# Optimization experiments

Hardware: AMD Instinct MI355X
Metric: run time of the kernel (lower is better)

The kernel has to match this reference:

```python
import jax, jax.numpy as jnp
import numpy as np

TAU = 0.5

def setup_inputs() -> dict:
    key = jax.random.key(0)
    ks = jax.random.split(key, 9)
    B, N, C, T, R = 32, 196, 768, 10, 16
    s = 0.02
    return {
        "x": jax.random.normal(ks[0], (B, N, C), jnp.float32),
        "W_qkv": jax.random.normal(ks[1], (3 * C, C), jnp.float32) * s,
        "b_qkv": jax.random.normal(ks[2], (3 * C,), jnp.float32) * s,
        "A_q": jax.random.normal(ks[3], (T, R, C), jnp.float32) * s,
        "B_q": jax.random.normal(ks[4], (T, C, R), jnp.float32) * s,
        "A_v": jax.random.normal(ks[5], (T, R, C), jnp.float32) * s,
        "B_v": jax.random.normal(ks[6], (T, C, R), jnp.float32) * s,
        "gate_logits_q": jax.random.normal(ks[7], (T,), jnp.float32),
        "gate_logits_v": jax.random.normal(ks[8], (T,), jnp.float32),
    }

def _fro(w):
    # Frobenius norm per task: w is [T, d1, d2]
    return jnp.sqrt(jnp.sum(w * w, axis=(1, 2)))

def _lora_branch(x, A, B, logits):
    # x: [B,N,C]; A: [T,R,C]; B: [T,C,R]; logits: [T]
    gate = jax.nn.softmax(logits / TAU)                      # soft gumbel gate, eval (no noise)
    scale = gate / (_fro(A) * _fro(B))                       # fuse 1/(||A||*||B||) with gate weight
    tmp = jnp.einsum('bnc,trc->tbnr', x, A)                  # low-rank projections, all tasks batched
    return jnp.einsum('tbnr,tcr,t->bnc', tmp, B, scale)      # up-project + weighted sum over tasks

def reference(x, W_qkv, b_qkv, A_q, B_q, A_v, B_v, gate_logits_q, gate_logits_v):
    C = x.shape[-1]
    qkv = jnp.einsum('bnc,dc->bnd', x, W_qkv) + b_qkv        # [B,N,3C]
    new_q = _lora_branch(x, A_q, B_q, gate_logits_q)
    new_v = _lora_branch(x, A_v, B_v, gate_logits_v)
    qkv = qkv.at[:, :, :C].add(new_q)
    qkv = qkv.at[:, :, 2 * C:].add(new_v)
    return qkv
```

## Files before the change

### kernel.cpp

```cpp
#include <hip/hip_runtime.h>

#define TAU_INV 2.0f

typedef unsigned short u16;
typedef short bf16x8 __attribute__((ext_vector_type(8)));
typedef float f32x4 __attribute__((ext_vector_type(4)));
typedef u16 u16x4v __attribute__((ext_vector_type(4)));
typedef u16 u16x8v __attribute__((ext_vector_type(8)));

typedef __attribute__((address_space(1))) const void GASV;
typedef __attribute__((address_space(3))) void LASV;
#define GLOAD16(gp, lp) __builtin_amdgcn_global_load_lds((GASV*)(gp), (LASV*)(lp), 16, 0, 0)

__device__ __forceinline__ u16 f2bf(float f) {
  unsigned u = __float_as_uint(f);
  u += 0x7FFFu + ((u >> 16) & 1u);
  return (u16)(u >> 16);
}

__global__ __launch_bounds__(256) void k_scales(
    const float* __restrict__ Aq, const float* __restrict__ Bq,
    const float* __restrict__ Av, const float* __restrict__ Bv,
    const float* __restrict__ lq, const float* __restrict__ lv,
    float* __restrict__ scales) {
  const int br = blockIdx.x / 10, t = blockIdx.x % 10;
  const float* __restrict__ A = br ? Av : Aq;
  const float* __restrict__ B = br ? Bv : Bq;
  const float* __restrict__ lg = br ? lv : lq;
  const int tid = threadIdx.x;
  const float4* A4 = (const float4*)(A + t * 12288);
  const float4* B4 = (const float4*)(B + t * 12288);
  float sA = 0.f, sB = 0.f;
  for (int i = tid; i < 3072; i += 256) {
    float4 a = A4[i];
    float4 b = B4[i];
    sA += a.x * a.x + a.y * a.y + a.z * a.z + a.w * a.w;
    sB += b.x * b.x + b.y * b.y + b.z * b.z + b.w * b.w;
  }
  for (int off = 32; off; off >>= 1) {
    sA += __shfl_down(sA, off);
    sB += __shfl_down(sB, off);
  }
  __shared__ float rA[4], rB[4];
  if ((tid & 63) == 0) { rA[tid >> 6] = sA; rB[tid >> 6] = sB; }
  __syncthreads();
  if (tid == 0) {
    sA = rA[0] + rA[1] + rA[2] + rA[3];
    sB = rB[0] + rB[1] + rB[2] + rB[3];
    float mx = -1e30f;
    for (int j = 0; j < 10; ++j) mx = fmaxf(mx, lg[j] * TAU_INV);
    float den = 0.f, num = 0.f;
    for (int j = 0; j < 10; ++j) {
      float e = __expf(lg[j] * TAU_INV - mx);
      den += e;
      if (j == t) num = e;
    }
    scales[br * 16 + t] = (num / den) * rsqrtf(sA) * rsqrtf(sB);
  }
}

__global__ __launch_bounds__(256) void k_xcvt(const float* __restrict__ x,
                                              u16* __restrict__ xb) {
  const int i = (blockIdx.x * 256 + threadIdx.x) * 8;
  float4 v0 = *(const float4*)(x + i);
  float4 v1 = *(const float4*)(x + i + 4);
  u16x8v o;
  o[0] = f2bf(v0.x); o[1] = f2bf(v0.y); o[2] = f2bf(v0.z); o[3] = f2bf(v0.w);
  o[4] = f2bf(v1.x); o[5] = f2bf(v1.y); o[6] = f2bf(v1.z); o[7] = f2bf(v1.w);
  *(u16x8v*)(xb + i) = o;
}

__global__ __launch_bounds__(256) void k_wmid(const float* __restrict__ W,
                                              u16* __restrict__ Weff) {
  const int i = 589824 + (blockIdx.x * 256 + threadIdx.x) * 8;
  float4 v0 = *(const float4*)(W + i);
  float4 v1 = *(const float4*)(W + i + 4);
  u16x8v o;
  o[0] = f2bf(v0.x); o[1] = f2bf(v0.y); o[2] = f2bf(v0.z); o[3] = f2bf(v0.w);
  o[4] = f2bf(v1.x); o[5] = f2bf(v1.y); o[6] = f2bf(v1.z); o[7] = f2bf(v1.w);
  *(u16x8v*)(Weff + i) = o;
}

__global__ __launch_bounds__(256) void k_dwgemm(
    const float* __restrict__ Aq, const float* __restrict__ Bq,
    const float* __restrict__ Av, const float* __restrict__ Bv,
    const float* __restrict__ W, const float* __restrict__ scales,
    u16* __restrict__ Weff) {
  const int bid = blockIdx.x;
  const int br = bid / 36, t36 = bid % 36;
  const int tm = t36 / 6, tn = t36 % 6;
  const float* __restrict__ A = br ? Av : Aq;
  const float* __restrict__ B = br ? Bv : Bq;
  const int d0 = tm * 128, c0 = tn * 128;
  const int rowbase = br ? 1536 : 0;
  __shared__ u16 As[128 * 32];
  __shared__ u16 Bs[128 * 32];
  const int tid = threadIdx.x;
  const int lane = tid & 63, w = tid >> 6, wm = w >> 1, wn = w & 1;
  const int lr = lane & 15, kb = lane >> 4;
  f32x4 acc[4][4];
#pragma unroll
  for (int i = 0; i < 4; ++i)
#pragma unroll
    for (int j = 0; j < 4; ++j)
#pragma unroll
      for (int e = 0; e < 4; ++e) acc[i][j][e] = 0.f;

  for (int it = 0; it < 5; ++it) {
    const int k0 = it * 32;
    if (it) __syncthreads();
#pragma unroll
    for (int i = 0; i < 4; ++i) {
      int q = tid + i * 256;
      int d = q >> 3;
      int k = (q & 7) * 4;
      int kg = k0 + k;
      int t = kg >> 4, r = kg & 15;
      float4 v = *(const float4*)(B + (t * 768 + d0 + d) * 16 + r);
      float s = scales[br * 16 + t];
      u16x4v o;
      o[0] = f2bf(v.x * s); o[1] = f2bf(v.y * s);
      o[2] = f2bf(v.z * s); o[3] = f2bf(v.w * s);
      *(u16x4v*)(As + q * 4) = o;
    }
#pragma unroll
    for (int i = 0; i < 4; ++i) {
      int q = tid + i * 256;
      int c = (q & 31) * 4;
      int kk = q >> 5;
      float4 v = *(const float4*)(A + (k0 + kk) * 768 + c0 + c);
      Bs[(c + 0) * 32 + kk] = f2bf(v.x);
      Bs[(c + 1) * 32 + kk] = f2bf(v.y);
      Bs[(c + 2) * 32 + kk] = f2bf(v.z);
      Bs[(c + 3) * 32 + kk] = f2bf(v.w);
    }
    __syncthreads();
    bf16x8 a[4], b[4];
#pragma unroll
    for (int i = 0; i < 4; ++i)
      a[i] = *(const bf16x8*)(As + (wm * 64 + i * 16 + lr) * 32 + kb * 8);
#pragma unroll
    for (int j = 0; j < 4; ++j)
      b[j] = *(const bf16x8*)(Bs + (wn * 64 + j * 16 + lr) * 32 + kb * 8);
#pragma unroll
    for (int i = 0; i < 4; ++i)
#pragma unroll
      for (int j = 0; j < 4; ++j)
        acc[i][j] = __builtin_amdgcn_mfma_f32_16x16x32_bf16(a[i], b[j], acc[i][j], 0, 0, 0);
  }
#pragma unroll
  for (int i = 0; i < 4; ++i)
#pragma unroll
    for (int jn = 0; jn < 4; ++jn)
#pragma unroll
      for (int j = 0; j < 4; ++j) {
        int row = rowbase + d0 + wm * 64 + i * 16 + kb * 4 + j;
        int col = c0 + wn * 64 + jn * 16 + lr;
        int g = row * 768 + col;
        Weff[g] = f2bf(W[g] + acc[i][jn][j]);
      }
}

__global__ __launch_bounds__(256, 3) void k_gemm(
    const u16* __restrict__ Xb,
    const u16* __restrict__ Wb,
    const float* __restrict__ bias,
    float* __restrict__ out) {
  const int bid = blockIdx.x;
  const int tn = bid % 18, tm = bid / 18;
  const int m0 = tm * 128, n0 = tn * 128;
  __shared__ u16 As[128 * 32];
  __shared__ u16 Bs[128 * 32];
  const int tid = threadIdx.x;
  const int lane = tid & 63, w = tid >> 6, wm = w >> 1, wn = w & 1;
  const int lr = lane & 15, kb = lane >> 4;
  f32x4 acc[4][4];
#pragma unroll
  for (int i = 0; i < 4; ++i)
#pragma unroll
    for (int j = 0; j < 4; ++j)
#pragma unroll
      for (int e = 0; e < 4; ++e) acc[i][j][e] = 0.f;

  const int r0 = tid >> 2;
  const int cb0 = (tid & 3) * 8;
  const u16* gA0 = Xb + (m0 + r0) * 768 + cb0;
  const u16* gA1 = Xb + (m0 + 64 + r0) * 768 + cb0;
  const u16* gB0 = Wb + (n0 + r0) * 768 + cb0;
  const u16* gB1 = Wb + (n0 + 64 + r0) * 768 + cb0;
  char* ldsA = (char*)As + (tid & 192) * 16;
  char* ldsB = (char*)Bs + (tid & 192) * 16;

  for (int kt = 0; kt < 24; ++kt) {
    const int ko = kt * 32;
    GLOAD16(gA0 + ko, ldsA);
    GLOAD16(gA1 + ko, ldsA + 4096);
    GLOAD16(gB0 + ko, ldsB);
    GLOAD16(gB1 + ko, ldsB + 4096);
    __syncthreads();
    bf16x8 a[4], b[4];
#pragma unroll
    for (int i = 0; i < 4; ++i)
      a[i] = *(const bf16x8*)(As + (wm * 64 + i * 16 + lr) * 32 + kb * 8);
#pragma unroll
    for (int j = 0; j < 4; ++j)
      b[j] = *(const bf16x8*)(Bs + (wn * 64 + j * 16 + lr) * 32 + kb * 8);
#pragma unroll
    for (int i = 0; i < 4; ++i)
#pragma unroll
      for (int j = 0; j < 4; ++j)
        acc[i][j] = __builtin_amdgcn_mfma_f32_16x16x32_bf16(a[i], b[j], acc[i][j], 0, 0, 0);
    __syncthreads();
  }

  float br4[4];
#pragma unroll
  for (int jn = 0; jn < 4; ++jn) br4[jn] = bias[n0 + wn * 64 + jn * 16 + lr];
#pragma unroll
  for (int i = 0; i < 4; ++i)
#pragma unroll
    for (int jn = 0; jn < 4; ++jn)
#pragma unroll
      for (int j = 0; j < 4; ++j) {
        int m = m0 + wm * 64 + i * 16 + kb * 4 + j;
        int n = n0 + wn * 64 + jn * 16 + lr;
        out[m * 2304 + n] = acc[i][jn][j] + br4[jn];
      }
}

extern "C" void kernel_launch(void* const* d_in, const int* in_sizes, int n_in,
                              void* d_out, int out_size, void* d_ws, size_t ws_size,
                              hipStream_t stream) {
  const float* x    = (const float*)d_in[0];
  const float* Wq   = (const float*)d_in[1];
  const float* bqkv = (const float*)d_in[2];
  const float* Aq   = (const float*)d_in[3];
  const float* Bq   = (const float*)d_in[4];
  const float* Av   = (const float*)d_in[5];
  const float* Bv   = (const float*)d_in[6];
  const float* lq   = (const float*)d_in[7];
  const float* lv   = (const float*)d_in[8];
  float* out = (float*)d_out;

  char* ws = (char*)d_ws;
  float* scales = (float*)ws;
  u16* xb   = (u16*)(ws + 256);
  u16* weff = (u16*)(ws + 256 + 9633792);

  k_scales<<<20, 256, 0, stream>>>(Aq, Bq, Av, Bv, lq, lv, scales);
  k_xcvt<<<2352, 256, 0, stream>>>(x, xb);
  k_wmid<<<288, 256, 0, stream>>>(Wq, weff);
  k_dwgemm<<<72, 256, 0, stream>>>(Aq, Bq, Av, Bv, Wq, scales, weff);
  k_gemm<<<882, 256, 0, stream>>>(xb, weff, bqkv, out);
}
```

Before: 173.2 us.

## Double-buffer GEMM LDS with XOR swizzle and merge prep kernels

The main GEMM now double-buffers its LDS tiles: it issues async global-to-LDS loads two k-steps ahead and uses vmcnt waits with raw barriers, so load latency overlaps the MFMA work. An XOR swizzle on the k-chunk index is meant to reduce LDS bank conflicts on the fragment reads. The x conversion and scale computation are merged into one launch, and the middle-W conversion is folded into the delta-W kernel, cutting the launch count from five to three. The doubled LDS use may lower occupancy under the 3-blocks-per-CU launch bound.

```diff
diff --git a/kernel.cpp b/kernel.cpp
--- a/kernel.cpp
+++ b/kernel.cpp
@@ -18,16 +18,29 @@
   return (u16)(u >> 16);
 }
 
-__global__ __launch_bounds__(256) void k_scales(
+__global__ __launch_bounds__(256) void k_prep(
+    const float* __restrict__ x, u16* __restrict__ xb,
     const float* __restrict__ Aq, const float* __restrict__ Bq,
     const float* __restrict__ Av, const float* __restrict__ Bv,
     const float* __restrict__ lq, const float* __restrict__ lv,
     float* __restrict__ scales) {
-  const int br = blockIdx.x / 10, t = blockIdx.x % 10;
+  const int bid = blockIdx.x;
+  const int tid = threadIdx.x;
+  if (bid < 2352) {
+    const int i = (bid * 256 + tid) * 8;
+    float4 v0 = *(const float4*)(x + i);
+    float4 v1 = *(const float4*)(x + i + 4);
+    u16x8v o;
+    o[0] = f2bf(v0.x); o[1] = f2bf(v0.y); o[2] = f2bf(v0.z); o[3] = f2bf(v0.w);
+    o[4] = f2bf(v1.x); o[5] = f2bf(v1.y); o[6] = f2bf(v1.z); o[7] = f2bf(v1.w);
+    *(u16x8v*)(xb + i) = o;
+    return;
+  }
+  const int sb = bid - 2352;
+  const int br = sb / 10, t = sb % 10;
   const float* __restrict__ A = br ? Av : Aq;
   const float* __restrict__ B = br ? Bv : Bq;
   const float* __restrict__ lg = br ? lv : lq;
-  const int tid = threadIdx.x;
   const float4* A4 = (const float4*)(A + t * 12288);
   const float4* B4 = (const float4*)(B + t * 12288);
   float sA = 0.f, sB = 0.f;
@@ -59,34 +72,27 @@
   }
 }
 
-__global__ __launch_bounds__(256) void k_xcvt(const float* __restrict__ x,
-                                              u16* __restrict__ xb) {
-  const int i = (blockIdx.x * 256 + threadIdx.x) * 8;
-  float4 v0 = *(const float4*)(x + i);
-  float4 v1 = *(const float4*)(x + i + 4);
-  u16x8v o;
-  o[0] = f2bf(v0.x); o[1] = f2bf(v0.y); o[2] = f2bf(v0.z); o[3] = f2bf(v0.w);
-  o[4] = f2bf(v1.x); o[5] = f2bf(v1.y); o[6] = f2bf(v1.z); o[7] = f2bf(v1.w);
-  *(u16x8v*)(xb + i) = o;
-}
-
-__global__ __launch_bounds__(256) void k_wmid(const float* __restrict__ W,
-                                              u16* __restrict__ Weff) {
-  const int i = 589824 + (blockIdx.x * 256 + threadIdx.x) * 8;
-  float4 v0 = *(const float4*)(W + i);
-  float4 v1 = *(const float4*)(W + i + 4);
-  u16x8v o;
-  o[0] = f2bf(v0.x); o[1] = f2bf(v0.y); o[2] = f2bf(v0.z); o[3] = f2bf(v0.w);
-  o[4] = f2bf(v1.x); o[5] = f2bf(v1.y); o[6] = f2bf(v1.z); o[7] = f2bf(v1.w);
-  *(u16x8v*)(Weff + i) = o;
-}
-
-__global__ __launch_bounds__(256) void k_dwgemm(
+__global__ __launch_bounds__(256) void k_dwpack(
     const float* __restrict__ Aq, const float* __restrict__ Bq,
     const float* __restrict__ Av, const float* __restrict__ Bv,
     const float* __restrict__ W, const float* __restrict__ scales,
     u16* __restrict__ Weff) {
   const int bid = blockIdx.x;
+  const int tid = threadIdx.x;
+  if (bid >= 72) {
+    const int base = 589824 + (bid - 72) * 16384;
+#pragma unroll
+    for (int it = 0; it < 8; ++it) {
+      const int i = base + (it * 256 + tid) * 8;
+      float4 v0 = *(const float4*)(W + i);
+      float4 v1 = *(const float4*)(W + i + 4);
+      u16x8v o;
+      o[0] = f2bf(v0.x); o[1] = f2bf(v0.y); o[2] = f2bf(v0.z); o[3] = f2bf(v0.w);
+      o[4] = f2bf(v1.x); o[5] = f2bf(v1.y); o[6] = f2bf(v1.z); o[7] = f2bf(v1.w);
+      *(u16x8v*)(Weff + i) = o;
+    }
+    return;
+  }
   const int br = bid / 36, t36 = bid % 36;
   const int tm = t36 / 6, tn = t36 % 6;
   const float* __restrict__ A = br ? Av : Aq;
@@ -95,7 +101,6 @@
   const int rowbase = br ? 1536 : 0;
   __shared__ u16 As[128 * 32];
   __shared__ u16 Bs[128 * 32];
-  const int tid = threadIdx.x;
   const int lane = tid & 63, w = tid >> 6, wm = w >> 1, wn = w & 1;
   const int lr = lane & 15, kb = lane >> 4;
   f32x4 acc[4][4];
@@ -169,11 +174,12 @@
   const int bid = blockIdx.x;
   const int tn = bid % 18, tm = bid / 18;
   const int m0 = tm * 128, n0 = tn * 128;
-  __shared__ u16 As[128 * 32];
-  __shared__ u16 Bs[128 * 32];
+  __shared__ u16 As[2][128 * 32];
+  __shared__ u16 Bs[2][128 * 32];
   const int tid = threadIdx.x;
   const int lane = tid & 63, w = tid >> 6, wm = w >> 1, wn = w & 1;
   const int lr = lane & 15, kb = lane >> 4;
+  const int kbx = (kb ^ (lr & 3)) * 8;
   f32x4 acc[4][4];
 #pragma unroll
   for (int i = 0; i < 4; ++i)
@@ -183,35 +189,58 @@
       for (int e = 0; e < 4; ++e) acc[i][j][e] = 0.f;
 
   const int r0 = tid >> 2;
-  const int cb0 = (tid & 3) * 8;
+  const int cb0 = ((tid & 3) ^ (r0 & 3)) * 8;
   const u16* gA0 = Xb + (m0 + r0) * 768 + cb0;
-  const u16* gA1 = Xb + (m0 + 64 + r0) * 768 + cb0;
+  const u16* gA1 = gA0 + 64 * 768;
   const u16* gB0 = Wb + (n0 + r0) * 768 + cb0;
-  const u16* gB1 = Wb + (n0 + 64 + r0) * 768 + cb0;
-  char* ldsA = (char*)As + (tid & 192) * 16;
-  char* ldsB = (char*)Bs + (tid & 192) * 16;
+  const u16* gB1 = gB0 + 64 * 768;
+  const int wbase = (tid & 192) * 16;
+
+#define STAGE(buf, kt)                                            \
+  {                                                               \
+    const int ko_ = (kt) * 32;                                    \
+    char* lA_ = (char*)&As[(buf)][0] + wbase;                     \
+    char* lB_ = (char*)&Bs[(buf)][0] + wbase;                     \
+    GLOAD16(gA0 + ko_, lA_);                                      \
+    GLOAD16(gA1 + ko_, lA_ + 4096);                               \
+    GLOAD16(gB0 + ko_, lB_);                                      \
+    GLOAD16(gB1 + ko_, lB_ + 4096);                               \
+  }
+
+  STAGE(0, 0)
+  STAGE(1, 1)
 
   for (int kt = 0; kt < 24; ++kt) {
-    const int ko = kt * 32;
-    GLOAD16(gA0 + ko, ldsA);
-    GLOAD16(gA1 + ko, ldsA + 4096);
-    GLOAD16(gB0 + ko, ldsB);
-    GLOAD16(gB1 + ko, ldsB + 4096);
-    __syncthreads();
-    bf16x8 a[4], b[4];
-#pragma unroll
-    for (int i = 0; i < 4; ++i)
-      a[i] = *(const bf16x8*)(As + (wm * 64 + i * 16 + lr) * 32 + kb * 8);
-#pragma unroll
-    for (int j = 0; j < 4; ++j)
-      b[j] = *(const bf16x8*)(Bs + (wn * 64 + j * 16 + lr) * 32 + kb * 8);
-#pragma unroll
-    for (int i = 0; i < 4; ++i)
+    const int cur = kt & 1;
+    if (kt < 23) {
+      asm volatile("s_waitcnt vmcnt(4)" ::: "memory");
+    } else {
+      asm volatile("s_waitcnt vmcnt(0)" ::: "memory");
+    }
+    __builtin_amdgcn_s_barrier();
+    asm volatile("" ::: "memory");
+    {
+      const u16* Ab = &As[cur][0];
+      const u16* Bb = &Bs[cur][0];
+      bf16x8 a[4], b[4];
+#pragma unroll
+      for (int i = 0; i < 4; ++i)
+        a[i] = *(const bf16x8*)(Ab + (wm * 64 + i * 16 + lr) * 32 + kbx);
 #pragma unroll
       for (int j = 0; j < 4; ++j)
-        acc[i][j] = __builtin_amdgcn_mfma_f32_16x16x32_bf16(a[i], b[j], acc[i][j], 0, 0, 0);
-    __syncthreads();
-  }
+        b[j] = *(const bf16x8*)(Bb + (wn * 64 + j * 16 + lr) * 32 + kbx);
+#pragma unroll
+      for (int i = 0; i < 4; ++i)
+#pragma unroll
+        for (int j = 0; j < 4; ++j)
+          acc[i][j] = __builtin_amdgcn_mfma_f32_16x16x32_bf16(a[i], b[j], acc[i][j], 0, 0, 0);
+    }
+    asm volatile("" ::: "memory");
+    __builtin_amdgcn_s_barrier();
+    asm volatile("" ::: "memory");
+    if (kt < 22) STAGE(cur, kt + 2)
+  }
+#undef STAGE
 
   float br4[4];
 #pragma unroll
@@ -247,9 +276,7 @@
   u16* xb   = (u16*)(ws + 256);
   u16* weff = (u16*)(ws + 256 + 9633792);
 
-  k_scales<<<20, 256, 0, stream>>>(Aq, Bq, Av, Bv, lq, lv, scales);
-  k_xcvt<<<2352, 256, 0, stream>>>(x, xb);
-  k_wmid<<<288, 256, 0, stream>>>(Wq, weff);
-  k_dwgemm<<<72, 256, 0, stream>>>(Aq, Bq, Av, Bv, Wq, scales, weff);
+  k_prep<<<2372, 256, 0, stream>>>(x, xb, Aq, Bq, Av, Bv, lq, lv, scales);
+  k_dwpack<<<108, 256, 0, stream>>>(Aq, Bq, Av, Bv, Wq, scales, weff);
   k_gemm<<<882, 256, 0, stream>>>(xb, weff, bqkv, out);
 }
```

Result: faster. 169.5 us (-2.1%).
